# Performance work log

Hardware: AMD Instinct MI355X
Metric: run time of the kernel (lower is better)

## Reference

```python
import jax, jax.numpy as jnp
import numpy as np

B, S, H = 4, 2048, 1024
E, F = 8, 4096
K = 2  # hardcoded top-k in the original forward


def setup_inputs() -> dict:
    key = jax.random.key(0)
    ks = jax.random.split(key, 8)
    scale = 0.02
    x = jax.random.normal(ks[0], (B, S, H), dtype=jnp.float32)
    Wr = jax.random.normal(ks[1], (H, E), dtype=jnp.float32) * scale
    br = jnp.zeros((E,), dtype=jnp.float32)
    W1 = jax.random.normal(ks[2], (E, H, F), dtype=jnp.float32) * scale
    b1 = jnp.zeros((E, F), dtype=jnp.float32)
    W2 = jax.random.normal(ks[3], (E, F, H), dtype=jnp.float32) * scale
    b2 = jnp.zeros((E, H), dtype=jnp.float32)
    return {"x": x, "Wr": Wr, "br": br, "W1": W1, "b1": b1, "W2": W2, "b2": b2}


def reference(x, Wr, br, W1, b1, W2, b2):
    # Router: [B,S,H] @ [H,E] -> [B,S,E]
    router_logits = jnp.einsum('bsh,he->bse', x, Wr) + br
    router_probs = jax.nn.softmax(router_logits, axis=-1)
    top_k_probs, top_k_indices = jax.lax.top_k(router_probs, K)
    top_k_probs = top_k_probs / jnp.sum(top_k_probs, axis=-1, keepdims=True)
    # NOTE: original code weights EVERY selected expert by the normalized top-1 prob.
    p0 = top_k_probs[..., 0]  # [B,S]

    combined = jnp.zeros((B, S, H), dtype=x.dtype)
    for e in range(E):
        mask = jnp.any(top_k_indices == e, axis=-1)  # [B,S]
        # Dense FFN (dropout deterministic => identity); gelu approximate (flax default)
        h = jax.nn.gelu(jnp.einsum('bsh,hf->bsf', x, W1[e]) + b1[e])
        y = jnp.einsum('bsf,fh->bsh', h, W2[e]) + b2[e]
        combined = combined + jnp.where(mask[..., None], y * p0[..., None], 0.0)
    return combined
```

## Files before the change

### kernel.cpp

```cpp
#include <hip/hip_runtime.h>
#include <hip/hip_bf16.h>


typedef __bf16 bf16;
typedef __attribute__((ext_vector_type(4))) __bf16 bf16x4;
typedef __attribute__((ext_vector_type(8))) __bf16 bf16x8;
typedef __attribute__((ext_vector_type(4))) float f32x4;

#define GLD16(g, l) __builtin_amdgcn_global_load_lds( \
    (__attribute__((address_space(1))) void*)(g),      \
    (__attribute__((address_space(3))) void*)(l), 16, 0, 0)

__device__ __forceinline__ float gelu_fast(float v) {
  float u = v * fmaf(v * v, 0.0713548162726f, 1.5957691216057308f);
  return v * __builtin_amdgcn_rcpf(1.0f + __expf(-u));
}

__global__ __launch_bounds__(256) void router_kernel(
    const float* __restrict__ x, const float* __restrict__ Wr,
    const float* __restrict__ br, int* __restrict__ e01,
    float* __restrict__ p0arr) {
  int wv = threadIdx.x >> 6;
  int l = threadIdx.x & 63;
  int t = blockIdx.x * 4 + wv;
  float acc[8];
#pragma unroll
  for (int e = 0; e < 8; e++) acc[e] = 0.f;
  const float* xr = x + (size_t)t * 1024;
#pragma unroll
  for (int i = 0; i < 16; i++) {
    int h = l + i * 64;
    float xv = xr[h];
    const float4* w4 = (const float4*)(Wr + h * 8);
    float4 wa = w4[0], wb = w4[1];
    acc[0] += xv * wa.x; acc[1] += xv * wa.y; acc[2] += xv * wa.z; acc[3] += xv * wa.w;
    acc[4] += xv * wb.x; acc[5] += xv * wb.y; acc[6] += xv * wb.z; acc[7] += xv * wb.w;
  }
#pragma unroll
  for (int e = 0; e < 8; e++) {
    float v = acc[e];
#pragma unroll
    for (int m = 1; m < 64; m <<= 1) v += __shfl_xor(v, m, 64);
    acc[e] = v + br[e];
  }
  int i1 = 0; float m1 = acc[0];
#pragma unroll
  for (int e = 1; e < 8; e++) { if (acc[e] > m1) { m1 = acc[e]; i1 = e; } }
  int i2 = -1; float m2 = -3.4e38f;
#pragma unroll
  for (int e = 0; e < 8; e++) { if (e != i1 && acc[e] > m2) { m2 = acc[e]; i2 = e; } }
  if (l == 0) {
    e01[t] = i1 | (i2 << 8);
    p0arr[t] = 1.0f / (1.0f + __expf(m2 - m1));
  }
}

__global__ __launch_bounds__(1024) void slots_kernel(
    const int* __restrict__ e01, int* __restrict__ off,
    int* __restrict__ slot1, int* __restrict__ slot2) {
  __shared__ int wtot[16];
  int tid = threadIdx.x;
  int l = tid & 63, wv = tid >> 6;
  int t0 = tid * 8;
  int i1[8], i2[8];
#pragma unroll
  for (int i = 0; i < 8; i++) {
    int ee = e01[t0 + i];
    i1[i] = ee & 255;
    i2[i] = (ee >> 8) & 255;
  }
  int running = 0;
  for (int e = 0; e < 8; e++) {
    int cthread = 0;
#pragma unroll
    for (int i = 0; i < 8; i++) cthread += (i1[i] == e) + (i2[i] == e);
    int inc = cthread;
#pragma unroll
    for (int d = 1; d < 64; d <<= 1) {
      int v = __shfl_up(inc, d, 64);
      if (l >= d) inc += v;
    }
    if (l == 63) wtot[wv] = inc;
    __syncthreads();
    int wbase = 0, total = 0;
#pragma unroll
    for (int w = 0; w < 16; w++) {
      int tw = wtot[w];
      wbase += (w < wv) ? tw : 0;
      total += tw;
    }
    int base = running + wbase + (inc - cthread);
#pragma unroll
    for (int i = 0; i < 8; i++) {
      if (i1[i] == e) { slot1[t0 + i] = base; base++; }
      if (i2[i] == e) { slot2[t0 + i] = base; base++; }
    }
    if (tid == 0) off[e] = running;
    running += (total + 127) & ~127;
    __syncthreads();
  }
  if (tid == 0) off[8] = running;
}

__global__ __launch_bounds__(256) void gather_kernel(
    const float* __restrict__ x, const int* __restrict__ slot1,
    const int* __restrict__ slot2, bf16* __restrict__ Xg) {
  int t = blockIdx.x;
  int s1 = slot1[t], s2 = slot2[t];
  float4 v = ((const float4*)(x + (size_t)t * 1024))[threadIdx.x];
  bf16x4 bv = { (bf16)v.x, (bf16)v.y, (bf16)v.z, (bf16)v.w };
  *(bf16x4*)(Xg + (size_t)s1 * 1024 + threadIdx.x * 4) = bv;
  *(bf16x4*)(Xg + (size_t)s2 * 1024 + threadIdx.x * 4) = bv;
}

__global__ __launch_bounds__(256) void tconv_kernel(
    const float* __restrict__ in, bf16* __restrict__ out, int R, int C) {
  __shared__ float tile[64][65];
  size_t base = (size_t)blockIdx.z * R * C;
  int gr0 = blockIdx.y * 64, gc0 = blockIdx.x * 64;
#pragma unroll
  for (int i = 0; i < 16; i++) {
    int idx = threadIdx.x + i * 256;
    int r = idx >> 6, c = idx & 63;
    tile[r][c] = in[base + (size_t)(gr0 + r) * C + gc0 + c];
  }
  __syncthreads();
  int rr0 = (threadIdx.x & 15) * 4;
#pragma unroll
  for (int i = 0; i < 4; i++) {
    int cc = (threadIdx.x >> 4) + i * 16;
    bf16x4 v = { (bf16)tile[rr0][cc], (bf16)tile[rr0 + 1][cc],
                 (bf16)tile[rr0 + 2][cc], (bf16)tile[rr0 + 3][cc] };
    *(bf16x4*)&out[base + (size_t)(gc0 + cc) * R + gr0 + rr0] = v;
  }
}

struct GemmCtx {
  const bf16* Abase;
  const bf16* Bbase;
  int K;
  int w, l, mbase, nbase;
};

__device__ __forceinline__ void gemm_mainloop(
    const GemmCtx& c, bf16* As0, bf16* As1, bf16* Bs0, bf16* Bs1,
    f32x4 acc[4][4]) {
  const int K = c.K;
  const int NT = K >> 5;
  int w = c.w, l = c.l;
  int gr = w * 32 + (l >> 2);
  int cg = (l & 3) ^ ((l >> 2) & 3);
  const bf16* Ap = c.Abase + (size_t)gr * K + cg * 8;
  const bf16* Bp = c.Bbase + (size_t)gr * K + cg * 8;
  int ldsoff = w * 1024 + l * 8;
  {
    GLD16(Ap, As0 + ldsoff);
    GLD16(Ap + (size_t)16 * K, As0 + ldsoff + 512);
    GLD16(Bp, Bs0 + ldsoff);
    GLD16(Bp + (size_t)16 * K, Bs0 + ldsoff + 512);
  }
  int arow[4], brow[4];
#pragma unroll
  for (int t = 0; t < 4; t++) {
    arow[t] = c.mbase + t * 16 + (l & 15);
    brow[t] = c.nbase + t * 16 + (l & 15);
  }
  int kc = l >> 4;
  for (int kt = 0; kt < NT; kt++) {
    __syncthreads();
    bf16* Ab = (kt & 1) ? As1 : As0;
    bf16* Bb = (kt & 1) ? Bs1 : Bs0;
    if (kt + 1 < NT) {
      bf16* An = (kt & 1) ? As0 : As1;
      bf16* Bn = (kt & 1) ? Bs0 : Bs1;
      const bf16* Ag = Ap + (size_t)(kt + 1) * 32;
      const bf16* Bg = Bp + (size_t)(kt + 1) * 32;
      GLD16(Ag, An + ldsoff);
      GLD16(Ag + (size_t)16 * K, An + ldsoff + 512);
      GLD16(Bg, Bn + ldsoff);
      GLD16(Bg + (size_t)16 * K, Bn + ldsoff + 512);
    }
    bf16x8 af[4], bfr[4];
#pragma unroll
    for (int t = 0; t < 4; t++) {
      int cgl = kc ^ (arow[t] & 3);
      af[t] = *(const bf16x8*)&Ab[arow[t] * 32 + cgl * 8];
    }
#pragma unroll
    for (int t = 0; t < 4; t++) {
      int cgl = kc ^ (brow[t] & 3);
      bfr[t] = *(const bf16x8*)&Bb[brow[t] * 32 + cgl * 8];
    }
#pragma unroll
    for (int mt = 0; mt < 4; mt++)
#pragma unroll
      for (int nt = 0; nt < 4; nt++)
        acc[mt][nt] = __builtin_amdgcn_mfma_f32_16x16x32_bf16(bfr[nt], af[mt], acc[mt][nt], 0, 0, 0);
  }
}

__global__ __launch_bounds__(256) void gemm1_kernel(
    const bf16* __restrict__ Xg, const bf16* __restrict__ W1t,
    const float* __restrict__ b1, bf16* __restrict__ hbuf,
    const int* __restrict__ off) {
  __shared__ bf16 As0[128 * 32], As1[128 * 32];
  __shared__ bf16 Bs0[128 * 32], Bs1[128 * 32];
  const int K = 1024;
  int b = blockIdx.x;
  int xcd = b & 7, j = b >> 3;
  int m_tile = xcd * 17 + (j >> 5);
  int n_tile = j & 31;
  int row0 = m_tile * 128;
  if (row0 >= off[8]) return;
  int e = 0;
#pragma unroll
  for (int i = 0; i < 8; i++) { if (row0 >= off[i + 1]) e = i + 1; }
  int tid = threadIdx.x;
  GemmCtx c;
  c.w = tid >> 6; c.l = tid & 63;
  c.mbase = (c.w >> 1) * 64; c.nbase = (c.w & 1) * 64;
  c.K = K;
  c.Abase = Xg + (size_t)row0 * K;
  c.Bbase = W1t + ((size_t)e * 4096 + n_tile * 128) * K;
  f32x4 acc[4][4];
#pragma unroll
  for (int a = 0; a < 4; a++)
#pragma unroll
    for (int bb = 0; bb < 4; bb++) acc[a][bb] = (f32x4){0.f, 0.f, 0.f, 0.f};
  gemm_mainloop(c, As0, As1, Bs0, Bs1, acc);
  int l = c.l;
  int mrow = l & 15, nq = (l >> 4) * 4;
  int gn0 = n_tile * 128 + c.nbase + nq;
  f32x4 bv[4];
#pragma unroll
  for (int nt = 0; nt < 4; nt++)
    bv[nt] = *(const f32x4*)(b1 + e * 4096 + gn0 + nt * 16);
#pragma unroll
  for (int mt = 0; mt < 4; mt++) {
    int gm = row0 + c.mbase + mt * 16 + mrow;
    bf16* rp = hbuf + (size_t)gm * 4096 + gn0;
#pragma unroll
    for (int nt = 0; nt < 4; nt++) {
      bf16x4 o;
#pragma unroll
      for (int jj = 0; jj < 4; jj++)
        o[jj] = (bf16)gelu_fast(acc[mt][nt][jj] + bv[nt][jj]);
      *(bf16x4*)(rp + nt * 16) = o;
    }
  }
}

__global__ __launch_bounds__(256) void gemm2_kernel(
    const bf16* __restrict__ hbuf, const bf16* __restrict__ W2t,
    const float* __restrict__ b2, bf16* __restrict__ yb,
    const int* __restrict__ off) {
  __shared__ bf16 As0[128 * 32], As1[128 * 32];
  __shared__ bf16 Bs0[128 * 32], Bs1[128 * 32];
  const int K = 4096;
  int b = blockIdx.x;
  int xcd = b & 7, j = b >> 3;
  int m_tile = xcd * 17 + (j >> 3);
  int n_tile = j & 7;
  int row0 = m_tile * 128;
  if (row0 >= off[8]) return;
  int e = 0;
#pragma unroll
  for (int i = 0; i < 8; i++) { if (row0 >= off[i + 1]) e = i + 1; }
  int tid = threadIdx.x;
  GemmCtx c;
  c.w = tid >> 6; c.l = tid & 63;
  c.mbase = (c.w >> 1) * 64; c.nbase = (c.w & 1) * 64;
  c.K = K;
  c.Abase = hbuf + (size_t)row0 * K;
  c.Bbase = W2t + ((size_t)e * 1024 + n_tile * 128) * K;
  f32x4 acc[4][4];
#pragma unroll
  for (int a = 0; a < 4; a++)
#pragma unroll
    for (int bb = 0; bb < 4; bb++) acc[a][bb] = (f32x4){0.f, 0.f, 0.f, 0.f};
  gemm_mainloop(c, As0, As1, Bs0, Bs1, acc);
  int l = c.l;
  int mrow = l & 15, nq = (l >> 4) * 4;
  int gn0 = n_tile * 128 + c.nbase + nq;
  f32x4 bv[4];
#pragma unroll
  for (int nt = 0; nt < 4; nt++)
    bv[nt] = *(const f32x4*)(b2 + e * 1024 + gn0 + nt * 16);
#pragma unroll
  for (int mt = 0; mt < 4; mt++) {
    int gm = row0 + c.mbase + mt * 16 + mrow;
    bf16* rp = yb + (size_t)gm * 1024 + gn0;
#pragma unroll
    for (int nt = 0; nt < 4; nt++) {
      bf16x4 o;
#pragma unroll
      for (int jj = 0; jj < 4; jj++)
        o[jj] = (bf16)(acc[mt][nt][jj] + bv[nt][jj]);
      *(bf16x4*)(rp + nt * 16) = o;
    }
  }
}

__global__ __launch_bounds__(256) void combine_kernel(
    const bf16* __restrict__ yb, const int* __restrict__ slot1,
    const int* __restrict__ slot2, const float* __restrict__ p0arr,
    float* __restrict__ out) {
  int t = blockIdx.x;
  int s1 = slot1[t], s2 = slot2[t];
  float w0 = p0arr[t];
  bf16x4 a = *(const bf16x4*)(yb + (size_t)s1 * 1024 + threadIdx.x * 4);
  bf16x4 b = *(const bf16x4*)(yb + (size_t)s2 * 1024 + threadIdx.x * 4);
  float4 o;
  o.x = w0 * ((float)a[0] + (float)b[0]);
  o.y = w0 * ((float)a[1] + (float)b[1]);
  o.z = w0 * ((float)a[2] + (float)b[2]);
  o.w = w0 * ((float)a[3] + (float)b[3]);
  *(float4*)(out + (size_t)t * 1024 + threadIdx.x * 4) = o;
}

extern "C" void kernel_launch(void* const* d_in, const int* in_sizes, int n_in,
                              void* d_out, int out_size, void* d_ws, size_t ws_size,
                              hipStream_t stream) {
  const float* x  = (const float*)d_in[0];
  const float* Wr = (const float*)d_in[1];
  const float* br = (const float*)d_in[2];
  const float* W1 = (const float*)d_in[3];
  const float* b1 = (const float*)d_in[4];
  const float* W2 = (const float*)d_in[5];
  const float* b2 = (const float*)d_in[6];
  float* out = (float*)d_out;

  char* ws = (char*)d_ws;
  int*   off   = (int*)(ws + 0);
  int*   e01   = (int*)(ws + 256);
  float* p0    = (float*)(ws + 33024);
  int*   slot1 = (int*)(ws + 65792);
  int*   slot2 = (int*)(ws + 98560);
  bf16*  Xg    = (bf16*)(ws + 131584);
  bf16*  W1t   = (bf16*)(ws + 35783168ULL);
  bf16*  W2t   = (bf16*)(ws + 102892032ULL);
  bf16*  hb    = (bf16*)(ws + 170000896ULL);
  bf16*  yb    = Xg;

  tconv_kernel<<<dim3(64, 16, 8), 256, 0, stream>>>(W1, W1t, 1024, 4096);
  tconv_kernel<<<dim3(16, 64, 8), 256, 0, stream>>>(W2, W2t, 4096, 1024);
  router_kernel<<<2048, 256, 0, stream>>>(x, Wr, br, e01, p0);
  slots_kernel<<<1, 1024, 0, stream>>>(e01, off, slot1, slot2);
  gather_kernel<<<8192, 256, 0, stream>>>(x, slot1, slot2, Xg);
  gemm1_kernel<<<4352, 256, 0, stream>>>(Xg, W1t, b1, hb, off);
  gemm2_kernel<<<1088, 256, 0, stream>>>(hb, W2t, b2, yb, off);
  combine_kernel<<<8192, 256, 0, stream>>>(yb, slot1, slot2, p0, out);
}
```

Measured before the change: 822.3 us.

## Rewrite expert GEMMs with 128x256 tiles, 8 waves, triple-buffered K=64 pipeline

Both expert GEMM kernels move from 128x128 tiles with 4 waves and a double-buffered K=32 loop to 128x256 tiles with 8 waves and a triple-buffered K=64 loop over 144KB of LDS. Global-to-LDS loads are split across two half-steps, with explicit vmcnt/lgkmcnt waits, raw barriers and s_setprio around the MFMA bursts, and the LDS layout gets a new XOR swizzle. The aim is more operand reuse per byte loaded, better hiding of load latency and fewer blocks. The cost is a single block per CU because of the LDS footprint, fewer blocks for gemm2, and hand-managed waitcnt counts that must stay exactly right.

```diff
diff --git a/kernel.cpp b/kernel.cpp
--- a/kernel.cpp
+++ b/kernel.cpp
@@ -135,168 +135,193 @@
   }
 }
 
-struct GemmCtx {
-  const bf16* Abase;
-  const bf16* Bbase;
-  int K;
-  int w, l, mbase, nbase;
-};
-
-__device__ __forceinline__ void gemm_mainloop(
-    const GemmCtx& c, bf16* As0, bf16* As1, bf16* Bs0, bf16* Bs1,
-    f32x4 acc[4][4]) {
-  const int K = c.K;
-  const int NT = K >> 5;
-  int w = c.w, l = c.l;
-  int gr = w * 32 + (l >> 2);
-  int cg = (l & 3) ^ ((l >> 2) & 3);
-  const bf16* Ap = c.Abase + (size_t)gr * K + cg * 8;
-  const bf16* Bp = c.Bbase + (size_t)gr * K + cg * 8;
-  int ldsoff = w * 1024 + l * 8;
+__device__ __forceinline__ void gemm8_mainloop(
+    const bf16* __restrict__ Abase, const bf16* __restrict__ Bbase,
+    int K, char* smem, f32x4 acc[4][4], int wr, int wc, int l) {
+  const int NT = K >> 6;
+  int tid = threadIdx.x;
+  size_t K2 = (size_t)K * 2;
+  const char* sA0; const char* sA1;
+  const char* sB0; const char* sB1; const char* sB2; const char* sB3;
   {
-    GLD16(Ap, As0 + ldsoff);
-    GLD16(Ap + (size_t)16 * K, As0 + ldsoff + 512);
-    GLD16(Bp, Bs0 + ldsoff);
-    GLD16(Bp + (size_t)16 * K, Bs0 + ldsoff + 512);
-  }
-  int arow[4], brow[4];
+    int p0 = tid * 16, r0 = p0 >> 7, c0 = p0 & 127;
+    int p1 = p0 + 8192, r1 = p1 >> 7, c1 = p1 & 127;
+    int p2 = p0 + 16384, r2 = p2 >> 7, c2 = p2 & 127;
+    int p3 = p0 + 24576, r3 = p3 >> 7, c3 = p3 & 127;
+    sA0 = (const char*)Abase + (size_t)r0 * K2 + (c0 ^ ((r0 & 7) << 4));
+    sA1 = (const char*)Abase + (size_t)r1 * K2 + (c1 ^ ((r1 & 7) << 4));
+    sB0 = (const char*)Bbase + (size_t)r0 * K2 + (c0 ^ ((r0 & 7) << 4));
+    sB1 = (const char*)Bbase + (size_t)r1 * K2 + (c1 ^ ((r1 & 7) << 4));
+    sB2 = (const char*)Bbase + (size_t)r2 * K2 + (c2 ^ ((r2 & 7) << 4));
+    sB3 = (const char*)Bbase + (size_t)r3 * K2 + (c3 ^ ((r3 & 7) << 4));
+  }
+  const int dA = tid * 16;
+  const int dB = 16384 + tid * 16;
+  int offA[4], offBf[4];
 #pragma unroll
   for (int t = 0; t < 4; t++) {
-    arow[t] = c.mbase + t * 16 + (l & 15);
-    brow[t] = c.nbase + t * 16 + (l & 15);
-  }
-  int kc = l >> 4;
+    int ra = wr * 64 + t * 16 + (l & 15);
+    offA[t] = ra * 128 + ((((l >> 4) << 4)) ^ ((ra & 7) << 4));
+    int rb = wc * 64 + t * 16 + (l & 15);
+    offBf[t] = 16384 + rb * 128 + ((((l >> 4) << 4)) ^ ((rb & 7) << 4));
+  }
+#pragma unroll
+  for (int t = 0; t < 2; t++) {
+    char* bu = smem + t * 49152;
+    GLD16(sA0 + t * 128, bu + dA);
+    GLD16(sA1 + t * 128, bu + dA + 8192);
+    GLD16(sB0 + t * 128, bu + dB);
+    GLD16(sB1 + t * 128, bu + dB + 8192);
+    GLD16(sB2 + t * 128, bu + dB + 16384);
+    GLD16(sB3 + t * 128, bu + dB + 24576);
+  }
+  sA0 += 256; sA1 += 256; sB0 += 256; sB1 += 256; sB2 += 256; sB3 += 256;
+  asm volatile("s_waitcnt vmcnt(6)" ::: "memory");
+  __builtin_amdgcn_s_barrier();
+  char* bc = smem;
+  char* bn2 = smem + 2 * 49152;
   for (int kt = 0; kt < NT; kt++) {
-    __syncthreads();
-    bf16* Ab = (kt & 1) ? As1 : As0;
-    bf16* Bb = (kt & 1) ? Bs1 : Bs0;
-    if (kt + 1 < NT) {
-      bf16* An = (kt & 1) ? As0 : As1;
-      bf16* Bn = (kt & 1) ? Bs0 : Bs1;
-      const bf16* Ag = Ap + (size_t)(kt + 1) * 32;
-      const bf16* Bg = Bp + (size_t)(kt + 1) * 32;
-      GLD16(Ag, An + ldsoff);
-      GLD16(Ag + (size_t)16 * K, An + ldsoff + 512);
-      GLD16(Bg, Bn + ldsoff);
-      GLD16(Bg + (size_t)16 * K, Bn + ldsoff + 512);
-    }
-    bf16x8 af[4], bfr[4];
+    bool st = (kt + 2) < NT;
+    bf16x8 af[4], bfv[4];
 #pragma unroll
     for (int t = 0; t < 4; t++) {
-      int cgl = kc ^ (arow[t] & 3);
-      af[t] = *(const bf16x8*)&Ab[arow[t] * 32 + cgl * 8];
-    }
+      af[t] = *(const bf16x8*)(bc + offA[t]);
+      bfv[t] = *(const bf16x8*)(bc + offBf[t]);
+    }
+    if (st) {
+      GLD16(sA0, bn2 + dA);
+      GLD16(sA1, bn2 + dA + 8192);
+      GLD16(sB0, bn2 + dB);
+    }
+    __builtin_amdgcn_s_barrier();
+    asm volatile("s_waitcnt lgkmcnt(0)" ::: "memory");
+    __builtin_amdgcn_s_setprio(1);
+#pragma unroll
+    for (int mf = 0; mf < 4; mf++)
+#pragma unroll
+      for (int nf = 0; nf < 4; nf++)
+        acc[mf][nf] = __builtin_amdgcn_mfma_f32_16x16x32_bf16(bfv[nf], af[mf], acc[mf][nf], 0, 0, 0);
+    __builtin_amdgcn_s_setprio(0);
+    __builtin_amdgcn_s_barrier();
 #pragma unroll
     for (int t = 0; t < 4; t++) {
-      int cgl = kc ^ (brow[t] & 3);
-      bfr[t] = *(const bf16x8*)&Bb[brow[t] * 32 + cgl * 8];
-    }
-#pragma unroll
-    for (int mt = 0; mt < 4; mt++)
-#pragma unroll
-      for (int nt = 0; nt < 4; nt++)
-        acc[mt][nt] = __builtin_amdgcn_mfma_f32_16x16x32_bf16(bfr[nt], af[mt], acc[mt][nt], 0, 0, 0);
-  }
-}
-
-__global__ __launch_bounds__(256) void gemm1_kernel(
+      af[t] = *(const bf16x8*)(bc + (offA[t] ^ 64));
+      bfv[t] = *(const bf16x8*)(bc + (offBf[t] ^ 64));
+    }
+    if (st) {
+      GLD16(sB1, bn2 + dB + 8192);
+      GLD16(sB2, bn2 + dB + 16384);
+      GLD16(sB3, bn2 + dB + 24576);
+      sA0 += 128; sA1 += 128; sB0 += 128; sB1 += 128; sB2 += 128; sB3 += 128;
+    }
+    __builtin_amdgcn_s_barrier();
+    asm volatile("s_waitcnt lgkmcnt(0)" ::: "memory");
+    __builtin_amdgcn_s_setprio(1);
+#pragma unroll
+    for (int mf = 0; mf < 4; mf++)
+#pragma unroll
+      for (int nf = 0; nf < 4; nf++)
+        acc[mf][nf] = __builtin_amdgcn_mfma_f32_16x16x32_bf16(bfv[nf], af[mf], acc[mf][nf], 0, 0, 0);
+    __builtin_amdgcn_s_setprio(0);
+    if (st) {
+      asm volatile("s_waitcnt vmcnt(6)" ::: "memory");
+    } else if (kt + 1 < NT) {
+      asm volatile("s_waitcnt vmcnt(0)" ::: "memory");
+    }
+    __builtin_amdgcn_s_barrier();
+    bc += 49152; if (bc == smem + 147456) bc = smem;
+    bn2 += 49152; if (bn2 == smem + 147456) bn2 = smem;
+  }
+}
+
+__global__ __launch_bounds__(512) void gemm1_kernel(
     const bf16* __restrict__ Xg, const bf16* __restrict__ W1t,
     const float* __restrict__ b1, bf16* __restrict__ hbuf,
     const int* __restrict__ off) {
-  __shared__ bf16 As0[128 * 32], As1[128 * 32];
-  __shared__ bf16 Bs0[128 * 32], Bs1[128 * 32];
-  const int K = 1024;
+  __shared__ __align__(16) char smem[147456];
   int b = blockIdx.x;
   int xcd = b & 7, j = b >> 3;
-  int m_tile = xcd * 17 + (j >> 5);
-  int n_tile = j & 31;
+  int m_tile = xcd * 17 + (j >> 4);
+  int n_tile = j & 15;
   int row0 = m_tile * 128;
   if (row0 >= off[8]) return;
   int e = 0;
 #pragma unroll
   for (int i = 0; i < 8; i++) { if (row0 >= off[i + 1]) e = i + 1; }
   int tid = threadIdx.x;
-  GemmCtx c;
-  c.w = tid >> 6; c.l = tid & 63;
-  c.mbase = (c.w >> 1) * 64; c.nbase = (c.w & 1) * 64;
-  c.K = K;
-  c.Abase = Xg + (size_t)row0 * K;
-  c.Bbase = W1t + ((size_t)e * 4096 + n_tile * 128) * K;
+  int w = tid >> 6, l = tid & 63;
+  int wr = w >> 2, wc = w & 3;
   f32x4 acc[4][4];
 #pragma unroll
   for (int a = 0; a < 4; a++)
 #pragma unroll
     for (int bb = 0; bb < 4; bb++) acc[a][bb] = (f32x4){0.f, 0.f, 0.f, 0.f};
-  gemm_mainloop(c, As0, As1, Bs0, Bs1, acc);
-  int l = c.l;
+  gemm8_mainloop(Xg + (size_t)row0 * 1024,
+                 W1t + ((size_t)e * 4096 + n_tile * 256) * 1024,
+                 1024, smem, acc, wr, wc, l);
   int mrow = l & 15, nq = (l >> 4) * 4;
-  int gn0 = n_tile * 128 + c.nbase + nq;
+  int gn0 = n_tile * 256 + wc * 64 + nq;
   f32x4 bv[4];
 #pragma unroll
-  for (int nt = 0; nt < 4; nt++)
-    bv[nt] = *(const f32x4*)(b1 + e * 4096 + gn0 + nt * 16);
-#pragma unroll
-  for (int mt = 0; mt < 4; mt++) {
-    int gm = row0 + c.mbase + mt * 16 + mrow;
+  for (int nf = 0; nf < 4; nf++)
+    bv[nf] = *(const f32x4*)(b1 + e * 4096 + gn0 + nf * 16);
+#pragma unroll
+  for (int mf = 0; mf < 4; mf++) {
+    int gm = row0 + wr * 64 + mf * 16 + mrow;
     bf16* rp = hbuf + (size_t)gm * 4096 + gn0;
 #pragma unroll
-    for (int nt = 0; nt < 4; nt++) {
+    for (int nf = 0; nf < 4; nf++) {
       bf16x4 o;
 #pragma unroll
       for (int jj = 0; jj < 4; jj++)
-        o[jj] = (bf16)gelu_fast(acc[mt][nt][jj] + bv[nt][jj]);
-      *(bf16x4*)(rp + nt * 16) = o;
-    }
-  }
-}
-
-__global__ __launch_bounds__(256) void gemm2_kernel(
+        o[jj] = (bf16)gelu_fast(acc[mf][nf][jj] + bv[nf][jj]);
+      *(bf16x4*)(rp + nf * 16) = o;
+    }
+  }
+}
+
+__global__ __launch_bounds__(512) void gemm2_kernel(
     const bf16* __restrict__ hbuf, const bf16* __restrict__ W2t,
     const float* __restrict__ b2, bf16* __restrict__ yb,
     const int* __restrict__ off) {
-  __shared__ bf16 As0[128 * 32], As1[128 * 32];
-  __shared__ bf16 Bs0[128 * 32], Bs1[128 * 32];
-  const int K = 4096;
+  __shared__ __align__(16) char smem[147456];
   int b = blockIdx.x;
   int xcd = b & 7, j = b >> 3;
-  int m_tile = xcd * 17 + (j >> 3);
-  int n_tile = j & 7;
+  int m_tile = xcd * 17 + (j >> 2);
+  int n_tile = j & 3;
   int row0 = m_tile * 128;
   if (row0 >= off[8]) return;
   int e = 0;
 #pragma unroll
   for (int i = 0; i < 8; i++) { if (row0 >= off[i + 1]) e = i + 1; }
   int tid = threadIdx.x;
-  GemmCtx c;
-  c.w = tid >> 6; c.l = tid & 63;
-  c.mbase = (c.w >> 1) * 64; c.nbase = (c.w & 1) * 64;
-  c.K = K;
-  c.Abase = hbuf + (size_t)row0 * K;
-  c.Bbase = W2t + ((size_t)e * 1024 + n_tile * 128) * K;
+  int w = tid >> 6, l = tid & 63;
+  int wr = w >> 2, wc = w & 3;
   f32x4 acc[4][4];
 #pragma unroll
   for (int a = 0; a < 4; a++)
 #pragma unroll
     for (int bb = 0; bb < 4; bb++) acc[a][bb] = (f32x4){0.f, 0.f, 0.f, 0.f};
-  gemm_mainloop(c, As0, As1, Bs0, Bs1, acc);
-  int l = c.l;
+  gemm8_mainloop(hbuf + (size_t)row0 * 4096,
+                 W2t + ((size_t)e * 1024 + n_tile * 256) * 4096,
+                 4096, smem, acc, wr, wc, l);
   int mrow = l & 15, nq = (l >> 4) * 4;
-  int gn0 = n_tile * 128 + c.nbase + nq;
+  int gn0 = n_tile * 256 + wc * 64 + nq;
   f32x4 bv[4];
 #pragma unroll
-  for (int nt = 0; nt < 4; nt++)
-    bv[nt] = *(const f32x4*)(b2 + e * 1024 + gn0 + nt * 16);
-#pragma unroll
-  for (int mt = 0; mt < 4; mt++) {
-    int gm = row0 + c.mbase + mt * 16 + mrow;
+  for (int nf = 0; nf < 4; nf++)
+    bv[nf] = *(const f32x4*)(b2 + e * 1024 + gn0 + nf * 16);
+#pragma unroll
+  for (int mf = 0; mf < 4; mf++) {
+    int gm = row0 + wr * 64 + mf * 16 + mrow;
     bf16* rp = yb + (size_t)gm * 1024 + gn0;
 #pragma unroll
-    for (int nt = 0; nt < 4; nt++) {
+    for (int nf = 0; nf < 4; nf++) {
       bf16x4 o;
 #pragma unroll
       for (int jj = 0; jj < 4; jj++)
-        o[jj] = (bf16)(acc[mt][nt][jj] + bv[nt][jj]);
-      *(bf16x4*)(rp + nt * 16) = o;
+        o[jj] = (bf16)(acc[mf][nf][jj] + bv[nf][jj]);
+      *(bf16x4*)(rp + nf * 16) = o;
     }
   }
 }
@@ -347,7 +372,7 @@
   router_kernel<<<2048, 256, 0, stream>>>(x, Wr, br, e01, p0);
   slots_kernel<<<1, 1024, 0, stream>>>(e01, off, slot1, slot2);
   gather_kernel<<<8192, 256, 0, stream>>>(x, slot1, slot2, Xg);
-  gemm1_kernel<<<4352, 256, 0, stream>>>(Xg, W1t, b1, hb, off);
-  gemm2_kernel<<<1088, 256, 0, stream>>>(hb, W2t, b2, yb, off);
+  gemm1_kernel<<<2176, 512, 0, stream>>>(Xg, W1t, b1, hb, off);
+  gemm2_kernel<<<544, 512, 0, stream>>>(hb, W2t, b2, yb, off);
   combine_kernel<<<8192, 256, 0, stream>>>(yb, slot1, slot2, p0, out);
 }
```

Result: faster. 758.2 us (-7.8%).
